# Kernel optimization log

Hardware: AMD Instinct MI355X
Metric: run time of the kernel (lower is better)

The kernel has to match this reference:

```python
import jax, jax.numpy as jnp
import numpy as np

QMAX = 127.0
EPS = 1e-12


def _smooth_quant(x, col_scale):
    """Per-row int8 quantization of (x * col_scale).
    Returns (q, row_scale): q holds integer values in [-127, 127] (kept in f32,
    exactly representable), row_scale is abs-max/127 per row."""
    xs = x * col_scale                                  # [R, K]
    row_scale = jnp.max(jnp.abs(xs), axis=-1) / QMAX    # [R]
    row_scale = jnp.maximum(row_scale, EPS)
    q = jnp.clip(jnp.round(xs / row_scale[:, None]), -QMAX, QMAX)
    return q, row_scale


def setup_inputs() -> dict:
    key = jax.random.key(0)
    k1, k2, k3 = jax.random.split(key, 3)
    B, S, K, N = 4, 8192, 1024, 1024
    input_ = jax.random.normal(k1, (B, S, K), dtype=jnp.float32)
    weight = jax.random.normal(k2, (N, K), dtype=jnp.float32) * 0.02
    bias = jax.random.normal(k3, (N,), dtype=jnp.float32) * 0.01
    return {"input": input_, "weight": weight, "bias": bias}


def reference(input, weight, bias):
    x2 = input.reshape(-1, input.shape[-1])             # [M, K]
    # SmoothQuant smoothing scale: sqrt(colmax(|x|) * colmax(|w|)), shape [K]
    in_max = jnp.max(jnp.abs(x2), axis=0)
    w_max = jnp.max(jnp.abs(weight), axis=0)
    smooth_scale = jnp.sqrt(jnp.maximum(in_max * w_max, EPS))
    # quantize activations divided by smooth_scale, weights multiplied by it
    x_q, x_s = _smooth_quant(x2, 1.0 / smooth_scale)    # [M,K], [M]
    w_q, w_s = _smooth_quant(weight, smooth_scale)      # [N,K], [N]
    # int8 matmul (emulated exactly in f32) + row/col dequant scales + bias
    acc = x_q @ w_q.T                                   # [M, N]
    out = acc * x_s[:, None] * w_s[None, :] + bias
    return out.reshape(*input.shape[:-1], weight.shape[0])
```

## Files before the change

### kernel.cpp

```cpp
#include <hip/hip_runtime.h>


typedef int v4i __attribute__((ext_vector_type(4)));

__device__ __forceinline__ void gld_lds16(const void* g, void* l) {
    __builtin_amdgcn_global_load_lds(
        (const __attribute__((address_space(1))) void*)g,
        (__attribute__((address_space(3))) void*)l,
        16, 0, 0);
}

__global__ __launch_bounds__(256) void colmax_part_kernel(const float* __restrict__ src,
                                                          int rows, int rpb, int K,
                                                          float* __restrict__ partial) {
    const int c = threadIdx.x * 4;
    int r0 = blockIdx.x * rpb;
    int r1 = r0 + rpb; if (r1 > rows) r1 = rows;
    float m0 = 0.f, m1 = 0.f, m2 = 0.f, m3 = 0.f;
    const float* p = src + (size_t)r0 * K + c;
#pragma unroll 4
    for (int r = r0; r < r1; ++r, p += K) {
        float4 v = *(const float4*)p;
        m0 = fmaxf(m0, fabsf(v.x));
        m1 = fmaxf(m1, fabsf(v.y));
        m2 = fmaxf(m2, fabsf(v.z));
        m3 = fmaxf(m3, fabsf(v.w));
    }
    float4 o; o.x = m0; o.y = m1; o.z = m2; o.w = m3;
    *(float4*)(partial + (size_t)blockIdx.x * K + c) = o;
}

__global__ void finalize_kernel(const float* __restrict__ px, int nx,
                                const float* __restrict__ pw, int nw,
                                float* __restrict__ smooth, float* __restrict__ inv_s, int K) {
    int c = blockIdx.x * blockDim.x + threadIdx.x;
    if (c >= K) return;
    float mx = 0.f, mw = 0.f;
    for (int r = 0; r < nx; ++r) mx = fmaxf(mx, px[(size_t)r * K + c]);
    for (int r = 0; r < nw; ++r) mw = fmaxf(mw, pw[(size_t)r * K + c]);
    float s = sqrtf(fmaxf(mx * mw, 1e-12f));
    smooth[c] = s;
    inv_s[c]  = 1.0f / s;
}

__global__ __launch_bounds__(256) void quant_rows_wave_kernel(
    const float* __restrict__ src, const float* __restrict__ colscale,
    signed char* __restrict__ q, float* __restrict__ rowscale, int K) {
    const int wave = threadIdx.x >> 6, lane = threadIdx.x & 63;
    const int row = blockIdx.x * 4 + wave;
    const float* srow = src + (size_t)row * K;
    float xs[16];
    float mv = 0.f;
#pragma unroll
    for (int i = 0; i < 4; ++i) {
        float4 v  = *(const float4*)(srow + i * 256 + lane * 4);
        float4 cs = *(const float4*)(colscale + i * 256 + lane * 4);
        xs[i*4+0] = v.x * cs.x; xs[i*4+1] = v.y * cs.y;
        xs[i*4+2] = v.z * cs.z; xs[i*4+3] = v.w * cs.w;
        mv = fmaxf(mv, fmaxf(fmaxf(fabsf(xs[i*4+0]), fabsf(xs[i*4+1])),
                             fmaxf(fabsf(xs[i*4+2]), fabsf(xs[i*4+3]))));
    }
#pragma unroll
    for (int off = 32; off > 0; off >>= 1)
        mv = fmaxf(mv, __shfl_xor(mv, off, 64));
    const float rs = fmaxf(mv / 127.0f, 1e-12f);
    signed char* qrow = q + (size_t)row * K;
#pragma unroll
    for (int i = 0; i < 4; ++i) {
        float q0 = fminf(fmaxf(rintf(xs[i*4+0] / rs), -127.f), 127.f);
        float q1 = fminf(fmaxf(rintf(xs[i*4+1] / rs), -127.f), 127.f);
        float q2 = fminf(fmaxf(rintf(xs[i*4+2] / rs), -127.f), 127.f);
        float q3 = fminf(fmaxf(rintf(xs[i*4+3] / rs), -127.f), 127.f);
        int b0 = (int)q0, b1 = (int)q1, b2 = (int)q2, b3 = (int)q3;
        unsigned packed = (unsigned)(b0 & 0xff) | ((unsigned)(b1 & 0xff) << 8)
                        | ((unsigned)(b2 & 0xff) << 16) | ((unsigned)(b3 & 0xff) << 24);
        *(unsigned*)(qrow + i * 256 + lane * 4) = packed;
    }
    if (lane == 0) rowscale[row] = rs;
}

__global__ __launch_bounds__(256) void gemm_i8_kernel(
    const signed char* __restrict__ Aq,
    const signed char* __restrict__ Bq,
    const float* __restrict__ xs,
    const float* __restrict__ wsc,
    const float* __restrict__ bias,
    float* __restrict__ out,
    int M, int N, int K) {
    __shared__ __align__(16) signed char As[128 * 64];
    __shared__ __align__(16) signed char Bs[128 * 64];

    const int tid  = threadIdx.x;
    const int lane = tid & 63;
    const int wave = tid >> 6;
    const int waveM = (wave >> 1) * 64;
    const int waveN = (wave & 1) * 64;

    const int bid = blockIdx.x;
    const int tile_m = (bid & 7) * 32 + (bid >> 6);
    const int tile_n = (bid >> 3) & 7;
    const int bm = tile_m * 128;
    const int bn = tile_n * 128;

    const int srow  = tid >> 2;
    const int qslot = tid & 3;
    const int gq    = (qslot ^ ((srow >> 1) & 3)) * 16;
    const int lbyte = qslot * 16;

    const signed char* aG0 = Aq + (size_t)(bm + srow) * K + gq;
    const signed char* aG1 = Aq + (size_t)(bm + 64 + srow) * K + gq;
    const signed char* bG0 = Bq + (size_t)(bn + srow) * K + gq;
    const signed char* bG1 = Bq + (size_t)(bn + 64 + srow) * K + gq;
    signed char* aL0 = As + srow * 64 + lbyte;
    signed char* aL1 = As + (64 + srow) * 64 + lbyte;
    signed char* bL0 = Bs + srow * 64 + lbyte;
    signed char* bL1 = Bs + (64 + srow) * 64 + lbyte;

    v4i acc[4][4] = {};

    const int fr = lane & 15;
    const int fp = (((lane >> 4) ^ ((fr >> 1) & 3))) * 16;

    for (int k0 = 0; k0 < K; k0 += 64) {
        __syncthreads();
        gld_lds16(aG0 + k0, aL0);
        gld_lds16(aG1 + k0, aL1);
        gld_lds16(bG0 + k0, bL0);
        gld_lds16(bG1 + k0, bL1);
        __syncthreads();

        v4i af[4], bf[4];
#pragma unroll
        for (int i = 0; i < 4; ++i)
            af[i] = *(const v4i*)(As + (waveM + i * 16 + fr) * 64 + fp);
#pragma unroll
        for (int j = 0; j < 4; ++j)
            bf[j] = *(const v4i*)(Bs + (waveN + j * 16 + fr) * 64 + fp);
#pragma unroll
        for (int i = 0; i < 4; ++i)
#pragma unroll
            for (int j = 0; j < 4; ++j)
                acc[i][j] = __builtin_amdgcn_mfma_i32_16x16x64_i8(af[i], bf[j], acc[i][j], 0, 0, 0);
    }

    const int orow0 = bm + waveM + (lane >> 4) * 4;
    const int ocol0 = bn + waveN + fr;
#pragma unroll
    for (int j = 0; j < 4; ++j) {
        const int col = ocol0 + j * 16;
        const float wn = wsc[col];
        const float bv = bias[col];
#pragma unroll
        for (int i = 0; i < 4; ++i) {
            const int rbase = orow0 + i * 16;
#pragma unroll
            for (int r = 0; r < 4; ++r) {
                const int row = rbase + r;
                float v = (float)acc[i][j][r] * xs[row];
                out[(size_t)row * N + col] = v * wn + bv;
            }
        }
    }
}

extern "C" void kernel_launch(void* const* d_in, const int* in_sizes, int n_in,
                              void* d_out, int out_size, void* d_ws, size_t ws_size,
                              hipStream_t stream) {
    const float* x    = (const float*)d_in[0];
    const float* w    = (const float*)d_in[1];
    const float* bias = (const float*)d_in[2];
    float* out = (float*)d_out;

    const int N = in_sizes[2];
    const int K = in_sizes[1] / N;
    const int M = in_sizes[0] / K;

    char* ws = (char*)d_ws;
    float* p1x       = (float*)(ws);
    float* p2x       = (float*)(ws + 2097152);
    float* pw        = (float*)(ws + 2162688);
    float* smooth    = (float*)(ws + 2228224);
    float* inv_s     = (float*)(ws + 2232320);
    float* w_s       = (float*)(ws + 2236416);
    float* x_s       = (float*)(ws + 2240512);
    signed char* x_q = (signed char*)(ws + 2371584);
    signed char* w_q = x_q + (size_t)M * K;

    colmax_part_kernel<<<512, 256, 0, stream>>>(x, M, 64, K, p1x);
    colmax_part_kernel<<<16, 256, 0, stream>>>(p1x, 512, 32, K, p2x);
    colmax_part_kernel<<<16, 256, 0, stream>>>(w, N, 64, K, pw);
    finalize_kernel<<<(K + 255) / 256, 256, 0, stream>>>(p2x, 16, pw, 16, smooth, inv_s, K);
    quant_rows_wave_kernel<<<N / 4, 256, 0, stream>>>(w, smooth, w_q, w_s, K);
    quant_rows_wave_kernel<<<M / 4, 256, 0, stream>>>(x, inv_s, x_q, x_s, K);
    gemm_i8_kernel<<<(M / 128) * (N / 128), 256, 0, stream>>>(x_q, w_q, x_s, w_s, bias, out, M, N, K);
}
```

Baseline: 338.5 us.

## Double-buffer LDS in int8 GEMM and vectorize quantization stores

```diff
diff --git a/kernel.cpp b/kernel.cpp
--- a/kernel.cpp
+++ b/kernel.cpp
@@ -18,7 +18,7 @@
     int r1 = r0 + rpb; if (r1 > rows) r1 = rows;
     float m0 = 0.f, m1 = 0.f, m2 = 0.f, m3 = 0.f;
     const float* p = src + (size_t)r0 * K + c;
-#pragma unroll 4
+#pragma unroll 8
     for (int r = r0; r < r1; ++r, p += K) {
         float4 v = *(const float4*)p;
         m0 = fmaxf(m0, fabsf(v.x));
@@ -48,13 +48,14 @@
     signed char* __restrict__ q, float* __restrict__ rowscale, int K) {
     const int wave = threadIdx.x >> 6, lane = threadIdx.x & 63;
     const int row = blockIdx.x * 4 + wave;
-    const float* srow = src + (size_t)row * K;
+    const float* srow = src + (size_t)row * K + lane * 16;
+    const float* crow = colscale + lane * 16;
     float xs[16];
     float mv = 0.f;
 #pragma unroll
     for (int i = 0; i < 4; ++i) {
-        float4 v  = *(const float4*)(srow + i * 256 + lane * 4);
-        float4 cs = *(const float4*)(colscale + i * 256 + lane * 4);
+        float4 v  = *(const float4*)(srow + i * 4);
+        float4 cs = *(const float4*)(crow + i * 4);
         xs[i*4+0] = v.x * cs.x; xs[i*4+1] = v.y * cs.y;
         xs[i*4+2] = v.z * cs.z; xs[i*4+3] = v.w * cs.w;
         mv = fmaxf(mv, fmaxf(fmaxf(fabsf(xs[i*4+0]), fabsf(xs[i*4+1])),
@@ -64,7 +65,7 @@
     for (int off = 32; off > 0; off >>= 1)
         mv = fmaxf(mv, __shfl_xor(mv, off, 64));
     const float rs = fmaxf(mv / 127.0f, 1e-12f);
-    signed char* qrow = q + (size_t)row * K;
+    unsigned pk[4];
 #pragma unroll
     for (int i = 0; i < 4; ++i) {
         float q0 = fminf(fmaxf(rintf(xs[i*4+0] / rs), -127.f), 127.f);
@@ -72,10 +73,10 @@
         float q2 = fminf(fmaxf(rintf(xs[i*4+2] / rs), -127.f), 127.f);
         float q3 = fminf(fmaxf(rintf(xs[i*4+3] / rs), -127.f), 127.f);
         int b0 = (int)q0, b1 = (int)q1, b2 = (int)q2, b3 = (int)q3;
-        unsigned packed = (unsigned)(b0 & 0xff) | ((unsigned)(b1 & 0xff) << 8)
-                        | ((unsigned)(b2 & 0xff) << 16) | ((unsigned)(b3 & 0xff) << 24);
-        *(unsigned*)(qrow + i * 256 + lane * 4) = packed;
-    }
+        pk[i] = (unsigned)(b0 & 0xff) | ((unsigned)(b1 & 0xff) << 8)
+              | ((unsigned)(b2 & 0xff) << 16) | ((unsigned)(b3 & 0xff) << 24);
+    }
+    *(uint4*)(q + (size_t)row * K + lane * 16) = make_uint4(pk[0], pk[1], pk[2], pk[3]);
     if (lane == 0) rowscale[row] = rs;
 }
 
@@ -87,8 +88,8 @@
     const float* __restrict__ bias,
     float* __restrict__ out,
     int M, int N, int K) {
-    __shared__ __align__(16) signed char As[128 * 64];
-    __shared__ __align__(16) signed char Bs[128 * 64];
+    __shared__ __align__(16) signed char As[2][128 * 64];
+    __shared__ __align__(16) signed char Bs[2][128 * 64];
 
     const int tid  = threadIdx.x;
     const int lane = tid & 63;
@@ -97,51 +98,60 @@
     const int waveN = (wave & 1) * 64;
 
     const int bid = blockIdx.x;
-    const int tile_m = (bid & 7) * 32 + (bid >> 6);
-    const int tile_n = (bid >> 3) & 7;
-    const int bm = tile_m * 128;
-    const int bn = tile_n * 128;
+    const int bm = ((bid & 7) * 32 + (bid >> 6)) * 128;
+    const int bn = ((bid >> 3) & 7) * 128;
 
     const int srow  = tid >> 2;
     const int qslot = tid & 3;
     const int gq    = (qslot ^ ((srow >> 1) & 3)) * 16;
-    const int lbyte = qslot * 16;
+    const int ldsOff = srow * 64 + qslot * 16;
 
     const signed char* aG0 = Aq + (size_t)(bm + srow) * K + gq;
     const signed char* aG1 = Aq + (size_t)(bm + 64 + srow) * K + gq;
     const signed char* bG0 = Bq + (size_t)(bn + srow) * K + gq;
     const signed char* bG1 = Bq + (size_t)(bn + 64 + srow) * K + gq;
-    signed char* aL0 = As + srow * 64 + lbyte;
-    signed char* aL1 = As + (64 + srow) * 64 + lbyte;
-    signed char* bL0 = Bs + srow * 64 + lbyte;
-    signed char* bL1 = Bs + (64 + srow) * 64 + lbyte;
 
     v4i acc[4][4] = {};
 
     const int fr = lane & 15;
-    const int fp = (((lane >> 4) ^ ((fr >> 1) & 3))) * 16;
-
-    for (int k0 = 0; k0 < K; k0 += 64) {
+    const int fp = ((lane >> 4) ^ ((fr >> 1) & 3)) * 16;
+
+#define STAGE(k0, b)                                   \
+    do {                                               \
+        gld_lds16(aG0 + (k0), &As[b][ldsOff]);         \
+        gld_lds16(aG1 + (k0), &As[b][ldsOff + 4096]);  \
+        gld_lds16(bG0 + (k0), &Bs[b][ldsOff]);         \
+        gld_lds16(bG1 + (k0), &Bs[b][ldsOff + 4096]);  \
+    } while (0)
+
+#define COMPUTE(b)                                                        \
+    do {                                                                  \
+        v4i af[4], bf[4];                                                 \
+        _Pragma("unroll")                                                 \
+        for (int i = 0; i < 4; ++i)                                       \
+            af[i] = *(const v4i*)&As[b][(waveM + i * 16 + fr) * 64 + fp]; \
+        _Pragma("unroll")                                                 \
+        for (int j = 0; j < 4; ++j)                                       \
+            bf[j] = *(const v4i*)&Bs[b][(waveN + j * 16 + fr) * 64 + fp]; \
+        _Pragma("unroll")                                                 \
+        for (int i = 0; i < 4; ++i)                                       \
+            _Pragma("unroll")                                             \
+            for (int j = 0; j < 4; ++j)                                   \
+                acc[i][j] = __builtin_amdgcn_mfma_i32_16x16x64_i8(        \
+                    af[i], bf[j], acc[i][j], 0, 0, 0);                    \
+    } while (0)
+
+    STAGE(0, 0);
+    for (int k0 = 0; k0 < K; k0 += 128) {
         __syncthreads();
-        gld_lds16(aG0 + k0, aL0);
-        gld_lds16(aG1 + k0, aL1);
-        gld_lds16(bG0 + k0, bL0);
-        gld_lds16(bG1 + k0, bL1);
+        if (k0 + 64 < K) STAGE(k0 + 64, 1);
+        COMPUTE(0);
         __syncthreads();
-
-        v4i af[4], bf[4];
-#pragma unroll
-        for (int i = 0; i < 4; ++i)
-            af[i] = *(const v4i*)(As + (waveM + i * 16 + fr) * 64 + fp);
-#pragma unroll
-        for (int j = 0; j < 4; ++j)
-            bf[j] = *(const v4i*)(Bs + (waveN + j * 16 + fr) * 64 + fp);
-#pragma unroll
-        for (int i = 0; i < 4; ++i)
-#pragma unroll
-            for (int j = 0; j < 4; ++j)
-                acc[i][j] = __builtin_amdgcn_mfma_i32_16x16x64_i8(af[i], bf[j], acc[i][j], 0, 0, 0);
-    }
+        if (k0 + 128 < K) STAGE(k0 + 128, 0);
+        COMPUTE(1);
+    }
+#undef STAGE
+#undef COMPUTE
 
     const int orow0 = bm + waveM + (lane >> 4) * 4;
     const int ocol0 = bn + waveN + fr;
@@ -177,17 +187,17 @@
 
     char* ws = (char*)d_ws;
     float* p1x       = (float*)(ws);
-    float* p2x       = (float*)(ws + 2097152);
-    float* pw        = (float*)(ws + 2162688);
-    float* smooth    = (float*)(ws + 2228224);
-    float* inv_s     = (float*)(ws + 2232320);
-    float* w_s       = (float*)(ws + 2236416);
-    float* x_s       = (float*)(ws + 2240512);
-    signed char* x_q = (signed char*)(ws + 2371584);
+    float* p2x       = (float*)(ws + 4194304);
+    float* pw        = (float*)(ws + 4259840);
+    float* smooth    = (float*)(ws + 4325376);
+    float* inv_s     = (float*)(ws + 4329472);
+    float* w_s       = (float*)(ws + 4333568);
+    float* x_s       = (float*)(ws + 4337664);
+    signed char* x_q = (signed char*)(ws + 4468736);
     signed char* w_q = x_q + (size_t)M * K;
 
-    colmax_part_kernel<<<512, 256, 0, stream>>>(x, M, 64, K, p1x);
-    colmax_part_kernel<<<16, 256, 0, stream>>>(p1x, 512, 32, K, p2x);
+    colmax_part_kernel<<<1024, 256, 0, stream>>>(x, M, 32, K, p1x);
+    colmax_part_kernel<<<16, 256, 0, stream>>>(p1x, 1024, 64, K, p2x);
     colmax_part_kernel<<<16, 256, 0, stream>>>(w, N, 64, K, pw);
     finalize_kernel<<<(K + 255) / 256, 256, 0, stream>>>(p2x, 16, pw, 16, smooth, inv_s, K);
     quant_rows_wave_kernel<<<N / 4, 256, 0, stream>>>(w, smooth, w_q, w_s, K);
```

Result: no change. 335.8 us (-0.8%).
